# Performance work log

Hardware: AMD Instinct MI355X
Metric: run time of the kernel (lower is better)

Reference implementation:

```python
import jax, jax.numpy as jnp
import numpy as np

N_NODES = 100000
N_EDGES = 1600000
IN_F = 128
H_F = 128
N_CLS = 8
N_LAYERS = 6


def setup_inputs() -> dict:
    key = jax.random.key(0)
    ks = jax.random.split(key, 8)
    scale = 1.0 / np.sqrt(H_F)
    return {
        "in_feat": jax.random.normal(ks[0], (N_NODES, IN_F), dtype=jnp.float32),
        "src": jax.random.randint(ks[1], (N_EDGES,), 0, N_NODES, dtype=jnp.int32),
        "dst": jax.random.randint(ks[2], (N_EDGES,), 0, N_NODES, dtype=jnp.int32),
        "edge_weight": jax.random.uniform(ks[3], (N_EDGES,), dtype=jnp.float32),
        "conv_W": jax.random.normal(ks[4], (N_LAYERS, H_F, H_F), dtype=jnp.float32) * scale,
        "conv_b": jnp.zeros((N_LAYERS, H_F), dtype=jnp.float32),
        "lin_W": jax.random.normal(ks[5], (H_F, N_CLS), dtype=jnp.float32) * scale,
        "lin_b": jnp.zeros((N_CLS,), dtype=jnp.float32),
    }


def _degree_norms(src, dst, n):
    ones = jnp.ones(src.shape[0], dtype=jnp.float32)
    out_deg = jax.ops.segment_sum(ones, src, num_segments=n)
    in_deg = jax.ops.segment_sum(ones, dst, num_segments=n)
    # DGL norm='both': clamp degrees to min 1, then ^-0.5 (structural degrees)
    norm_src = jnp.power(jnp.maximum(out_deg, 1.0), -0.5)[:, None]  # [N,1]
    norm_dst = jnp.power(jnp.maximum(in_deg, 1.0), -0.5)[:, None]   # [N,1]
    return norm_src, norm_dst


def _graph_conv(x, W, b, src, dst, ew, norm_src, norm_dst):
    # linear commutes with (linear) aggregation; apply weight first
    h = (x @ W) * norm_src                     # [N,F]
    msg = h[src] * ew[:, None]                 # [E,F] gather * edge weight
    agg = jax.ops.segment_sum(msg, dst, num_segments=x.shape[0])
    return agg * norm_dst + b


def reference(in_feat, src, dst, edge_weight, conv_W, conv_b, lin_W, lin_b):
    norm_src, norm_dst = _degree_norms(src, dst, in_feat.shape[0])
    h = in_feat
    for i in range(N_LAYERS):
        h = jax.nn.leaky_relu(
            _graph_conv(h, conv_W[i], conv_b[i], src, dst, edge_weight, norm_src, norm_dst),
            negative_slope=0.01,
        )
    return h @ lin_W + lin_b
```

## Files before the change

### kernel.cpp

```cpp
#include <hip/hip_runtime.h>
#include <math.h>

#define N_NODES 100000
#define N_EDGES 1600000
#define HF 128
#define N_CLS 8
#define N_LAYERS 6
#define TILE_N 64
#define SCAN_B 1024
#define SCAN_NB ((N_NODES + SCAN_B - 1) / SCAN_B)
#define HBINS 8192
#define HCHUNK ((N_NODES + HBINS - 1) / HBINS)
#define HSLICE 8

__global__ void deg_rank_kernel(const int* __restrict__ dst,
                                int* __restrict__ ind, int* __restrict__ rank) {
    int e = blockIdx.x * blockDim.x + threadIdx.x;
    if (e < N_EDGES) {
        rank[e] = atomicAdd(&ind[dst[e]], 1);
    }
}

__global__ __launch_bounds__(1024) void outdeg_hist_kernel(const int* __restrict__ src,
                                                           int* __restrict__ outd) {
    __shared__ int hist[HBINS];
    int chunk = blockIdx.x;
    int slice = blockIdx.y;
    int lo = chunk * HBINS;
    int hi = lo + HBINS;
    for (int i = threadIdx.x; i < HBINS; i += 1024) hist[i] = 0;
    __syncthreads();
    const int4* s4 = (const int4*)src;
    const int n4 = N_EDGES / 4;
    int per = (n4 + HSLICE - 1) / HSLICE;
    int beg = slice * per;
    int end = beg + per; if (end > n4) end = n4;
    for (int i = beg + threadIdx.x; i < end; i += 1024) {
        int4 v = s4[i];
        if (v.x >= lo && v.x < hi) atomicAdd(&hist[v.x - lo], 1);
        if (v.y >= lo && v.y < hi) atomicAdd(&hist[v.y - lo], 1);
        if (v.z >= lo && v.z < hi) atomicAdd(&hist[v.z - lo], 1);
        if (v.w >= lo && v.w < hi) atomicAdd(&hist[v.w - lo], 1);
    }
    __syncthreads();
    for (int i = threadIdx.x; i < HBINS; i += 1024) {
        int c = hist[i];
        if (c != 0 && lo + i < N_NODES) atomicAdd(&outd[lo + i], c);
    }
}

__global__ void norm_kernel(const int* __restrict__ outd, const int* __restrict__ ind,
                            float* __restrict__ ns, float* __restrict__ nd) {
    int n = blockIdx.x * blockDim.x + threadIdx.x;
    if (n < N_NODES) {
        int od = outd[n]; if (od < 1) od = 1;
        int id = ind[n];  if (id < 1) id = 1;
        ns[n] = rsqrtf((float)od);
        nd[n] = rsqrtf((float)id);
    }
}

__global__ __launch_bounds__(SCAN_B) void scan1_kernel(const int* __restrict__ deg,
                                                       int* __restrict__ incl,
                                                       int* __restrict__ bsum) {
    __shared__ int buf[SCAN_B];
    int t = threadIdx.x;
    int g = blockIdx.x * SCAN_B + t;
    int v = (g < N_NODES) ? deg[g] : 0;
    buf[t] = v;
    __syncthreads();
    #pragma unroll
    for (int off = 1; off < SCAN_B; off <<= 1) {
        int add = (t >= off) ? buf[t - off] : 0;
        __syncthreads();
        buf[t] += add;
        __syncthreads();
    }
    if (g < N_NODES) incl[g] = buf[t];
    if (t == SCAN_B - 1) bsum[blockIdx.x] = buf[t];
}

__global__ __launch_bounds__(128) void scan2_kernel(int* __restrict__ bsum) {
    __shared__ int buf[128];
    int t = threadIdx.x;
    buf[t] = (t < SCAN_NB) ? bsum[t] : 0;
    __syncthreads();
    #pragma unroll
    for (int off = 1; off < 128; off <<= 1) {
        int add = (t >= off) ? buf[t - off] : 0;
        __syncthreads();
        buf[t] += add;
        __syncthreads();
    }
    if (t < SCAN_NB) bsum[t] = buf[t];
}

__global__ __launch_bounds__(SCAN_B) void scan3_kernel(const int* __restrict__ deg,
                                                       const int* __restrict__ incl,
                                                       const int* __restrict__ bsum,
                                                       int* __restrict__ row_ptr) {
    int t = threadIdx.x;
    int g = blockIdx.x * SCAN_B + t;
    if (g < N_NODES) {
        int off = (blockIdx.x > 0) ? bsum[blockIdx.x - 1] : 0;
        row_ptr[g] = off + incl[g] - deg[g];
    }
    if (g == 0) row_ptr[N_NODES] = bsum[SCAN_NB - 1];
}

__global__ void scatter2_kernel(const int* __restrict__ src, const int* __restrict__ dst,
                                const float* __restrict__ ew, const float* __restrict__ ns,
                                const float* __restrict__ nd, const int* __restrict__ row_ptr,
                                const int* __restrict__ rank, float2* __restrict__ esw) {
    int e = blockIdx.x * blockDim.x + threadIdx.x;
    if (e < N_EDGES) {
        int s = src[e];
        int d = dst[e];
        int pos = row_ptr[d] + rank[e];
        esw[pos] = make_float2(__int_as_float(s), ew[e] * ns[s] * nd[d]);
    }
}

__global__ __launch_bounds__(256) void gemm_kernel(const float* __restrict__ X,
                                                   const float* __restrict__ W,
                                                   float* __restrict__ Y) {
    __shared__ float Xs[TILE_N][HF];
    int tid = threadIdx.x;
    int nodeBase = blockIdx.x * TILE_N;

    for (int i = tid; i < TILE_N * (HF / 4); i += 256) {
        int r = i >> 5;
        int c = i & 31;
        int n = nodeBase + r;
        float4 v = make_float4(0.f, 0.f, 0.f, 0.f);
        if (n < N_NODES) v = ((const float4*)(X + (size_t)n * HF))[c];
        ((float4*)(&Xs[r][0]))[c] = v;
    }
    __syncthreads();

    int tx = tid & 31;
    int ty = tid >> 5;

    float acc[8][4];
    #pragma unroll
    for (int i = 0; i < 8; i++)
        #pragma unroll
        for (int j = 0; j < 4; j++) acc[i][j] = 0.f;

    const float4* W4 = (const float4*)W;

    for (int k4 = 0; k4 < HF / 4; k4++) {
        float4 wv0 = W4[(k4 * 4 + 0) * 32 + tx];
        float4 wv1 = W4[(k4 * 4 + 1) * 32 + tx];
        float4 wv2 = W4[(k4 * 4 + 2) * 32 + tx];
        float4 wv3 = W4[(k4 * 4 + 3) * 32 + tx];
        #pragma unroll
        for (int i = 0; i < 8; i++) {
            float4 xv = ((const float4*)(&Xs[ty + 8 * i][0]))[k4];
            acc[i][0] += xv.x * wv0.x; acc[i][1] += xv.x * wv0.y;
            acc[i][2] += xv.x * wv0.z; acc[i][3] += xv.x * wv0.w;
            acc[i][0] += xv.y * wv1.x; acc[i][1] += xv.y * wv1.y;
            acc[i][2] += xv.y * wv1.z; acc[i][3] += xv.y * wv1.w;
            acc[i][0] += xv.z * wv2.x; acc[i][1] += xv.z * wv2.y;
            acc[i][2] += xv.z * wv2.z; acc[i][3] += xv.z * wv2.w;
            acc[i][0] += xv.w * wv3.x; acc[i][1] += xv.w * wv3.y;
            acc[i][2] += xv.w * wv3.z; acc[i][3] += xv.w * wv3.w;
        }
    }

    #pragma unroll
    for (int i = 0; i < 8; i++) {
        int n = nodeBase + ty + 8 * i;
        if (n < N_NODES) {
            float4 o = make_float4(acc[i][0], acc[i][1], acc[i][2], acc[i][3]);
            ((float4*)(Y + (size_t)n * HF))[tx] = o;
        }
    }
}

__global__ __launch_bounds__(256) void agg_kernel(const float* __restrict__ hl,
                                                  const int* __restrict__ row_ptr,
                                                  const float2* __restrict__ esw,
                                                  const float* __restrict__ bias,
                                                  float* __restrict__ out) {
    int node = blockIdx.x * 4 + (threadIdx.x >> 6);
    if (node >= N_NODES) return;
    int lane = threadIdx.x & 63;
    int half = lane >> 5;
    int fl = lane & 31;

    int beg = row_ptr[node];
    int end = row_ptr[node + 1];
    float ax = 0.f, ay = 0.f, az = 0.f, aw = 0.f;

    int i = beg;
    for (; i + 2 <= end; i += 2) {
        float2 p = esw[i + half];
        int s = __float_as_int(p.x);
        float4 v = ((const float4*)(hl + (size_t)s * HF))[fl];
        ax += v.x * p.y; ay += v.y * p.y;
        az += v.z * p.y; aw += v.w * p.y;
    }
    if (i < end && half == 0) {
        float2 p = esw[i];
        int s = __float_as_int(p.x);
        float4 v = ((const float4*)(hl + (size_t)s * HF))[fl];
        ax += v.x * p.y; ay += v.y * p.y;
        az += v.z * p.y; aw += v.w * p.y;
    }

    ax += __shfl_xor(ax, 32);
    ay += __shfl_xor(ay, 32);
    az += __shfl_xor(az, 32);
    aw += __shfl_xor(aw, 32);

    if (half == 0) {
        float4 bb = ((const float4*)bias)[fl];
        float ox = ax + bb.x;
        float oy = ay + bb.y;
        float oz = az + bb.z;
        float ow = aw + bb.w;
        ox = (ox > 0.f) ? ox : 0.01f * ox;
        oy = (oy > 0.f) ? oy : 0.01f * oy;
        oz = (oz > 0.f) ? oz : 0.01f * oz;
        ow = (ow > 0.f) ? ow : 0.01f * ow;
        ((float4*)(out + (size_t)node * HF))[fl] = make_float4(ox, oy, oz, ow);
    }
}

__global__ __launch_bounds__(256) void proj_kernel(const float* __restrict__ h,
                                                   const float* __restrict__ W,
                                                   const float* __restrict__ b,
                                                   float* __restrict__ out) {
    int node = blockIdx.x * (blockDim.x >> 6) + (threadIdx.x >> 6);
    if (node >= N_NODES) return;
    int lane = threadIdx.x & 63;

    float2 v = *(const float2*)(h + (size_t)node * HF + lane * 2);
    float acc[N_CLS];
    #pragma unroll
    for (int c = 0; c < N_CLS; c++) {
        acc[c] = v.x * W[(lane * 2) * N_CLS + c] + v.y * W[(lane * 2 + 1) * N_CLS + c];
    }
    #pragma unroll
    for (int off = 32; off > 0; off >>= 1) {
        #pragma unroll
        for (int c = 0; c < N_CLS; c++) acc[c] += __shfl_down(acc[c], off);
    }
    if (lane == 0) {
        #pragma unroll
        for (int c = 0; c < N_CLS; c++) out[(size_t)node * N_CLS + c] = acc[c] + b[c];
    }
}

extern "C" void kernel_launch(void* const* d_in, const int* in_sizes, int n_in,
                              void* d_out, int out_size, void* d_ws, size_t ws_size,
                              hipStream_t stream) {
    const float* in_feat = (const float*)d_in[0];
    const int*   src     = (const int*)d_in[1];
    const int*   dst     = (const int*)d_in[2];
    const float* ew      = (const float*)d_in[3];
    const float* conv_W  = (const float*)d_in[4];
    const float* conv_b  = (const float*)d_in[5];
    const float* lin_W   = (const float*)d_in[6];
    const float* lin_b   = (const float*)d_in[7];
    float* out = (float*)d_out;

    char* p = (char*)d_ws;
    float* hA = (float*)p;        p += (size_t)N_NODES * HF * sizeof(float);
    float* hB = (float*)p;        p += (size_t)N_NODES * HF * sizeof(float);
    float2* esw = (float2*)p;     p += (size_t)N_EDGES * sizeof(float2);
    int*   row_ptr = (int*)p;     p += ((size_t)N_NODES + 8) * sizeof(int);
    int*   out_deg = (int*)p;     p += (size_t)N_NODES * sizeof(int);
    int*   in_deg = (int*)p;      p += (size_t)N_NODES * sizeof(int);
    float* norm_src = (float*)p;  p += (size_t)N_NODES * sizeof(float);
    float* norm_dst = (float*)p;  p += (size_t)N_NODES * sizeof(float);
    int*   incl = (int*)p;        p += (size_t)N_NODES * sizeof(int);
    int*   bsum = (int*)p;        p += 256 * sizeof(int);
    int*   rank = (int*)hB;
    (void)p; (void)ws_size; (void)in_sizes; (void)n_in; (void)out_size;

    hipMemsetAsync(out_deg, 0, (size_t)N_NODES * sizeof(int), stream);
    hipMemsetAsync(in_deg, 0, (size_t)N_NODES * sizeof(int), stream);

    int egrid = (N_EDGES + 255) / 256;
    int ngrid = (N_NODES + 255) / 256;

    deg_rank_kernel<<<egrid, 256, 0, stream>>>(dst, in_deg, rank);
    outdeg_hist_kernel<<<dim3(HCHUNK, HSLICE), 1024, 0, stream>>>(src, out_deg);
    norm_kernel<<<ngrid, 256, 0, stream>>>(out_deg, in_deg, norm_src, norm_dst);
    scan1_kernel<<<SCAN_NB, SCAN_B, 0, stream>>>(in_deg, incl, bsum);
    scan2_kernel<<<1, 128, 0, stream>>>(bsum);
    scan3_kernel<<<SCAN_NB, SCAN_B, 0, stream>>>(in_deg, incl, bsum, row_ptr);
    scatter2_kernel<<<egrid, 256, 0, stream>>>(src, dst, ew, norm_src, norm_dst,
                                               row_ptr, rank, esw);

    int ggrid = (N_NODES + TILE_N - 1) / TILE_N;
    int agrid = (N_NODES + 3) / 4;

    const float* cur = in_feat;
    for (int l = 0; l < N_LAYERS; l++) {
        gemm_kernel<<<ggrid, 256, 0, stream>>>(cur, conv_W + (size_t)l * HF * HF, hB);
        agg_kernel<<<agrid, 256, 0, stream>>>(hB, row_ptr, esw,
                                              conv_b + (size_t)l * HF, hA);
        cur = hA;
    }
    proj_kernel<<<agrid, 256, 0, stream>>>(hA, lin_W, lin_b, out);
}
```

Baseline: 1.304 ms.

## Replace FP32 GEMM with bf16x3 split-precision MFMA matrix cores

The per-layer dense transform moves from scalar FP32 FMA to MFMA bf16 instructions. Each operand is split into three bf16 parts (hi/mid/lo) and six cross-product passes are accumulated to keep accuracy close to FP32. Weights are pre-split and transposed once by a new prep kernel, and activations are split on the fly into a swizzled shared-memory layout. This adds conversion work, triples the shared-memory footprint and writes output with scalar strided stores.

Measured after the change: 1.364 ms. 1.05x slower.

```diff
diff --git a/kernel.cpp b/kernel.cpp
--- a/kernel.cpp
+++ b/kernel.cpp
@@ -13,6 +13,20 @@
 #define HCHUNK ((N_NODES + HBINS - 1) / HBINS)
 #define HSLICE 8
 
+typedef __attribute__((ext_vector_type(8))) short bf16x8;
+typedef __attribute__((ext_vector_type(4))) float f32x4;
+
+__device__ __forceinline__ unsigned short bf_rne(float x) {
+    unsigned u = __float_as_uint(x);
+    u += 0x7FFFu + ((u >> 16) & 1u);
+    return (unsigned short)(u >> 16);
+}
+__device__ __forceinline__ float bf_to_f(unsigned short h) {
+    return __uint_as_float(((unsigned)h) << 16);
+}
+
+#define LDSOFF(row, k) (((row) << 8) + (((((k) >> 3) << 4) ^ (((row) & 7) << 4))) + (((k) & 7) << 1))
+
 __global__ void deg_rank_kernel(const int* __restrict__ dst,
                                 int* __restrict__ ind, int* __restrict__ rank) {
     int e = blockIdx.x * blockDim.x + threadIdx.x;
@@ -121,59 +135,109 @@
     }
 }
 
-__global__ __launch_bounds__(256) void gemm_kernel(const float* __restrict__ X,
-                                                   const float* __restrict__ W,
-                                                   float* __restrict__ Y) {
-    __shared__ float Xs[TILE_N][HF];
+__global__ __launch_bounds__(256) void wprep_kernel(const float* __restrict__ conv_W,
+                                                    unsigned short* __restrict__ wt) {
+    int l = blockIdx.y;
+    int idx = blockIdx.x * 256 + threadIdx.x;
+    int k = idx >> 7, f = idx & 127;
+    float x = conv_W[(size_t)l * 16384 + idx];
+    unsigned short h0 = bf_rne(x);
+    float r1 = x - bf_to_f(h0);
+    unsigned short h1 = bf_rne(r1);
+    float r2 = r1 - bf_to_f(h1);
+    unsigned short h2 = bf_rne(r2);
+    size_t base = (size_t)l * 3 * 16384 + (size_t)f * 128 + k;
+    wt[base]         = h0;
+    wt[base + 16384] = h1;
+    wt[base + 32768] = h2;
+}
+
+__global__ __launch_bounds__(256) void gemm_mfma_kernel(const float* __restrict__ X,
+                                                        const unsigned short* __restrict__ Wt,
+                                                        float* __restrict__ Y) {
+    __shared__ unsigned short Xb[3][TILE_N * HF];
     int tid = threadIdx.x;
     int nodeBase = blockIdx.x * TILE_N;
 
-    for (int i = tid; i < TILE_N * (HF / 4); i += 256) {
-        int r = i >> 5;
-        int c = i & 31;
+    for (int it = 0; it < 8; it++) {
+        int idx = tid + it * 256;
+        int r = idx >> 5;
+        int c = idx & 31;
         int n = nodeBase + r;
         float4 v = make_float4(0.f, 0.f, 0.f, 0.f);
         if (n < N_NODES) v = ((const float4*)(X + (size_t)n * HF))[c];
-        ((float4*)(&Xs[r][0]))[c] = v;
-    }
-    __syncthreads();
-
-    int tx = tid & 31;
-    int ty = tid >> 5;
-
-    float acc[8][4];
-    #pragma unroll
-    for (int i = 0; i < 8; i++)
-        #pragma unroll
-        for (int j = 0; j < 4; j++) acc[i][j] = 0.f;
-
-    const float4* W4 = (const float4*)W;
-
-    for (int k4 = 0; k4 < HF / 4; k4++) {
-        float4 wv0 = W4[(k4 * 4 + 0) * 32 + tx];
-        float4 wv1 = W4[(k4 * 4 + 1) * 32 + tx];
-        float4 wv2 = W4[(k4 * 4 + 2) * 32 + tx];
-        float4 wv3 = W4[(k4 * 4 + 3) * 32 + tx];
-        #pragma unroll
-        for (int i = 0; i < 8; i++) {
-            float4 xv = ((const float4*)(&Xs[ty + 8 * i][0]))[k4];
-            acc[i][0] += xv.x * wv0.x; acc[i][1] += xv.x * wv0.y;
-            acc[i][2] += xv.x * wv0.z; acc[i][3] += xv.x * wv0.w;
-            acc[i][0] += xv.y * wv1.x; acc[i][1] += xv.y * wv1.y;
-            acc[i][2] += xv.y * wv1.z; acc[i][3] += xv.y * wv1.w;
-            acc[i][0] += xv.z * wv2.x; acc[i][1] += xv.z * wv2.y;
-            acc[i][2] += xv.z * wv2.z; acc[i][3] += xv.z * wv2.w;
-            acc[i][0] += xv.w * wv3.x; acc[i][1] += xv.w * wv3.y;
-            acc[i][2] += xv.w * wv3.z; acc[i][3] += xv.w * wv3.w;
+        float vv[4] = {v.x, v.y, v.z, v.w};
+        unsigned short h0[4], h1[4], h2[4];
+        #pragma unroll
+        for (int j = 0; j < 4; j++) {
+            float x = vv[j];
+            h0[j] = bf_rne(x);
+            float r1 = x - bf_to_f(h0[j]);
+            h1[j] = bf_rne(r1);
+            float r2 = r1 - bf_to_f(h1[j]);
+            h2[j] = bf_rne(r2);
         }
-    }
-
-    #pragma unroll
-    for (int i = 0; i < 8; i++) {
-        int n = nodeBase + ty + 8 * i;
-        if (n < N_NODES) {
-            float4 o = make_float4(acc[i][0], acc[i][1], acc[i][2], acc[i][3]);
-            ((float4*)(Y + (size_t)n * HF))[tx] = o;
+        int boff = LDSOFF(r, c * 4) >> 1;
+        *(uint2*)&Xb[0][boff] = *(uint2*)h0;
+        *(uint2*)&Xb[1][boff] = *(uint2*)h1;
+        *(uint2*)&Xb[2][boff] = *(uint2*)h2;
+    }
+    __syncthreads();
+
+    int lane = tid & 63;
+    int wv = tid >> 6;
+    int lrow = lane & 15;
+    int lk8 = lane >> 4;
+
+    f32x4 acc[4][2];
+    #pragma unroll
+    for (int m = 0; m < 4; m++)
+        #pragma unroll
+        for (int n = 0; n < 2; n++)
+            acc[m][n] = (f32x4){0.f, 0.f, 0.f, 0.f};
+
+    const int pa[6] = {0, 0, 1, 0, 1, 2};
+    const int pb[6] = {0, 1, 0, 2, 1, 0};
+
+    #pragma unroll
+    for (int p = 0; p < 6; p++) {
+        const unsigned short* xb = Xb[pa[p]];
+        const unsigned short* wb = Wt + (size_t)pb[p] * 16384;
+        #pragma unroll
+        for (int ks = 0; ks < 4; ks++) {
+            int k0 = ks * 32 + lk8 * 8;
+            bf16x8 afr[4];
+            #pragma unroll
+            for (int m = 0; m < 4; m++) {
+                int row = m * 16 + lrow;
+                afr[m] = *(const bf16x8*)&xb[LDSOFF(row, k0) >> 1];
+            }
+            bf16x8 bfr[2];
+            #pragma unroll
+            for (int n = 0; n < 2; n++) {
+                int col = wv * 32 + n * 16 + lrow;
+                bfr[n] = *(const bf16x8*)&wb[col * 128 + k0];
+            }
+            #pragma unroll
+            for (int m = 0; m < 4; m++)
+                #pragma unroll
+                for (int n = 0; n < 2; n++)
+                    acc[m][n] = __builtin_amdgcn_mfma_f32_16x16x32_bf16(
+                        afr[m], bfr[n], acc[m][n], 0, 0, 0);
+        }
+    }
+
+    #pragma unroll
+    for (int m = 0; m < 4; m++) {
+        int rowBase = nodeBase + m * 16 + lk8 * 4;
+        #pragma unroll
+        for (int n = 0; n < 2; n++) {
+            int feat = wv * 32 + n * 16 + lrow;
+            #pragma unroll
+            for (int rr = 0; rr < 4; rr++) {
+                int nd = rowBase + rr;
+                if (nd < N_NODES) Y[(size_t)nd * HF + feat] = acc[m][n][rr];
+            }
         }
     }
 }
@@ -277,6 +341,7 @@
     float* norm_dst = (float*)p;  p += (size_t)N_NODES * sizeof(float);
     int*   incl = (int*)p;        p += (size_t)N_NODES * sizeof(int);
     int*   bsum = (int*)p;        p += 256 * sizeof(int);
+    unsigned short* wt = (unsigned short*)p; p += (size_t)N_LAYERS * 3 * 16384 * sizeof(unsigned short);
     int*   rank = (int*)hB;
     (void)p; (void)ws_size; (void)in_sizes; (void)n_in; (void)out_size;
 
@@ -294,13 +359,14 @@
     scan3_kernel<<<SCAN_NB, SCAN_B, 0, stream>>>(in_deg, incl, bsum, row_ptr);
     scatter2_kernel<<<egrid, 256, 0, stream>>>(src, dst, ew, norm_src, norm_dst,
                                                row_ptr, rank, esw);
+    wprep_kernel<<<dim3(64, N_LAYERS), 256, 0, stream>>>(conv_W, wt);
 
     int ggrid = (N_NODES + TILE_N - 1) / TILE_N;
     int agrid = (N_NODES + 3) / 4;
 
     const float* cur = in_feat;
     for (int l = 0; l < N_LAYERS; l++) {
-        gemm_kernel<<<ggrid, 256, 0, stream>>>(cur, conv_W + (size_t)l * HF * HF, hB);
+        gemm_mfma_kernel<<<ggrid, 256, 0, stream>>>(cur, wt + (size_t)l * 3 * 16384, hB);
         agg_kernel<<<agrid, 256, 0, stream>>>(hB, row_ptr, esw,
                                               conv_b + (size_t)l * HF, hA);
         cur = hA;
```

## Sub-bin CSR edges by source range to improve gather locality

Applied to the files above, without the earlier changes.

Edges in each destination row are now bucketed into 16 bins by source-node range, using a counting sort over N_NODES*16 bins, so each node's neighbors are visited roughly in ascending source order. The aim is better L2 locality for the feature gathers in the aggregation kernel across all six layers. In exchange the preprocessing scan grows sixteenfold (1.6M bins, with a serial chunked second-level scan), and bins and incl reuse the hA buffer.

After: 1.336 ms. 2.5% more time.

```diff
diff --git a/kernel.cpp b/kernel.cpp
--- a/kernel.cpp
+++ b/kernel.cpp
@@ -7,17 +7,23 @@
 #define N_CLS 8
 #define N_LAYERS 6
 #define TILE_N 64
+#define NS 16
+#define SDIV 6250
+#define NBINS (N_NODES * NS)
 #define SCAN_B 1024
-#define SCAN_NB ((N_NODES + SCAN_B - 1) / SCAN_B)
+#define SCAN_NB1 ((NBINS + SCAN_B - 1) / SCAN_B)
 #define HBINS 8192
 #define HCHUNK ((N_NODES + HBINS - 1) / HBINS)
 #define HSLICE 8
 
-__global__ void deg_rank_kernel(const int* __restrict__ dst,
-                                int* __restrict__ ind, int* __restrict__ rank) {
+__global__ void deg_rank_kernel(const int* __restrict__ src, const int* __restrict__ dst,
+                                int* __restrict__ bins, int* __restrict__ rank) {
     int e = blockIdx.x * blockDim.x + threadIdx.x;
     if (e < N_EDGES) {
-        rank[e] = atomicAdd(&ind[dst[e]], 1);
+        int s = src[e];
+        int d = dst[e];
+        int bin = d * NS + s / SDIV;
+        rank[e] = atomicAdd(&bins[bin], 1);
     }
 }
 
@@ -49,12 +55,13 @@
     }
 }
 
-__global__ void norm_kernel(const int* __restrict__ outd, const int* __restrict__ ind,
+__global__ void norm_kernel(const int* __restrict__ outd, const int* __restrict__ sptr,
                             float* __restrict__ ns, float* __restrict__ nd) {
     int n = blockIdx.x * blockDim.x + threadIdx.x;
     if (n < N_NODES) {
         int od = outd[n]; if (od < 1) od = 1;
-        int id = ind[n];  if (id < 1) id = 1;
+        int id = sptr[(n + 1) * NS] - sptr[n * NS];
+        if (id < 1) id = 1;
         ns[n] = rsqrtf((float)od);
         nd[n] = rsqrtf((float)id);
     }
@@ -66,7 +73,7 @@
     __shared__ int buf[SCAN_B];
     int t = threadIdx.x;
     int g = blockIdx.x * SCAN_B + t;
-    int v = (g < N_NODES) ? deg[g] : 0;
+    int v = (g < NBINS) ? deg[g] : 0;
     buf[t] = v;
     __syncthreads();
     #pragma unroll
@@ -76,47 +83,58 @@
         buf[t] += add;
         __syncthreads();
     }
-    if (g < N_NODES) incl[g] = buf[t];
+    if (g < NBINS) incl[g] = buf[t];
     if (t == SCAN_B - 1) bsum[blockIdx.x] = buf[t];
 }
 
-__global__ __launch_bounds__(128) void scan2_kernel(int* __restrict__ bsum) {
-    __shared__ int buf[128];
+__global__ __launch_bounds__(1024) void scan2_kernel(int* __restrict__ bsum) {
+    __shared__ int buf[1024];
+    __shared__ int carry_s;
     int t = threadIdx.x;
-    buf[t] = (t < SCAN_NB) ? bsum[t] : 0;
-    __syncthreads();
-    #pragma unroll
-    for (int off = 1; off < 128; off <<= 1) {
-        int add = (t >= off) ? buf[t - off] : 0;
-        __syncthreads();
-        buf[t] += add;
-        __syncthreads();
-    }
-    if (t < SCAN_NB) bsum[t] = buf[t];
+    if (t == 0) carry_s = 0;
+    __syncthreads();
+    for (int base = 0; base < SCAN_NB1; base += 1024) {
+        int v = (base + t < SCAN_NB1) ? bsum[base + t] : 0;
+        buf[t] = v;
+        __syncthreads();
+        #pragma unroll
+        for (int off = 1; off < 1024; off <<= 1) {
+            int add = (t >= off) ? buf[t - off] : 0;
+            __syncthreads();
+            buf[t] += add;
+            __syncthreads();
+        }
+        int incl = buf[t];
+        int carry = carry_s;
+        if (base + t < SCAN_NB1) bsum[base + t] = carry + incl;
+        __syncthreads();
+        if (t == 1023) carry_s = carry + incl;
+        __syncthreads();
+    }
 }
 
 __global__ __launch_bounds__(SCAN_B) void scan3_kernel(const int* __restrict__ deg,
                                                        const int* __restrict__ incl,
                                                        const int* __restrict__ bsum,
-                                                       int* __restrict__ row_ptr) {
+                                                       int* __restrict__ sptr) {
     int t = threadIdx.x;
     int g = blockIdx.x * SCAN_B + t;
-    if (g < N_NODES) {
+    if (g < NBINS) {
         int off = (blockIdx.x > 0) ? bsum[blockIdx.x - 1] : 0;
-        row_ptr[g] = off + incl[g] - deg[g];
-    }
-    if (g == 0) row_ptr[N_NODES] = bsum[SCAN_NB - 1];
+        sptr[g] = off + incl[g] - deg[g];
+    }
+    if (g == 0) sptr[NBINS] = bsum[SCAN_NB1 - 1];
 }
 
 __global__ void scatter2_kernel(const int* __restrict__ src, const int* __restrict__ dst,
                                 const float* __restrict__ ew, const float* __restrict__ ns,
-                                const float* __restrict__ nd, const int* __restrict__ row_ptr,
+                                const float* __restrict__ nd, const int* __restrict__ sptr,
                                 const int* __restrict__ rank, float2* __restrict__ esw) {
     int e = blockIdx.x * blockDim.x + threadIdx.x;
     if (e < N_EDGES) {
         int s = src[e];
         int d = dst[e];
-        int pos = row_ptr[d] + rank[e];
+        int pos = sptr[d * NS + s / SDIV] + rank[e];
         esw[pos] = make_float2(__int_as_float(s), ew[e] * ns[s] * nd[d]);
     }
 }
@@ -179,7 +197,7 @@
 }
 
 __global__ __launch_bounds__(256) void agg_kernel(const float* __restrict__ hl,
-                                                  const int* __restrict__ row_ptr,
+                                                  const int* __restrict__ sptr,
                                                   const float2* __restrict__ esw,
                                                   const float* __restrict__ bias,
                                                   float* __restrict__ out) {
@@ -189,8 +207,8 @@
     int half = lane >> 5;
     int fl = lane & 31;
 
-    int beg = row_ptr[node];
-    int end = row_ptr[node + 1];
+    int beg = sptr[node * NS];
+    int end = sptr[node * NS + NS];
     float ax = 0.f, ay = 0.f, az = 0.f, aw = 0.f;
 
     int i = beg;
@@ -270,30 +288,31 @@
     float* hA = (float*)p;        p += (size_t)N_NODES * HF * sizeof(float);
     float* hB = (float*)p;        p += (size_t)N_NODES * HF * sizeof(float);
     float2* esw = (float2*)p;     p += (size_t)N_EDGES * sizeof(float2);
-    int*   row_ptr = (int*)p;     p += ((size_t)N_NODES + 8) * sizeof(int);
+    int*   sptr = (int*)p;        p += ((size_t)NBINS + 8) * sizeof(int);
+    int*   bsum = (int*)p;        p += ((size_t)SCAN_NB1 + 8) * sizeof(int);
     int*   out_deg = (int*)p;     p += (size_t)N_NODES * sizeof(int);
-    int*   in_deg = (int*)p;      p += (size_t)N_NODES * sizeof(int);
     float* norm_src = (float*)p;  p += (size_t)N_NODES * sizeof(float);
     float* norm_dst = (float*)p;  p += (size_t)N_NODES * sizeof(float);
-    int*   incl = (int*)p;        p += (size_t)N_NODES * sizeof(int);
-    int*   bsum = (int*)p;        p += 256 * sizeof(int);
-    int*   rank = (int*)hB;
     (void)p; (void)ws_size; (void)in_sizes; (void)n_in; (void)out_size;
 
+    int* rank = (int*)hB;
+    int* bins = (int*)hA;
+    int* incl = (int*)hA + 2000000;
+
+    hipMemsetAsync(bins, 0, (size_t)NBINS * sizeof(int), stream);
     hipMemsetAsync(out_deg, 0, (size_t)N_NODES * sizeof(int), stream);
-    hipMemsetAsync(in_deg, 0, (size_t)N_NODES * sizeof(int), stream);
 
     int egrid = (N_EDGES + 255) / 256;
     int ngrid = (N_NODES + 255) / 256;
 
-    deg_rank_kernel<<<egrid, 256, 0, stream>>>(dst, in_deg, rank);
+    deg_rank_kernel<<<egrid, 256, 0, stream>>>(src, dst, bins, rank);
     outdeg_hist_kernel<<<dim3(HCHUNK, HSLICE), 1024, 0, stream>>>(src, out_deg);
-    norm_kernel<<<ngrid, 256, 0, stream>>>(out_deg, in_deg, norm_src, norm_dst);
-    scan1_kernel<<<SCAN_NB, SCAN_B, 0, stream>>>(in_deg, incl, bsum);
-    scan2_kernel<<<1, 128, 0, stream>>>(bsum);
-    scan3_kernel<<<SCAN_NB, SCAN_B, 0, stream>>>(in_deg, incl, bsum, row_ptr);
+    scan1_kernel<<<SCAN_NB1, SCAN_B, 0, stream>>>(bins, incl, bsum);
+    scan2_kernel<<<1, 1024, 0, stream>>>(bsum);
+    scan3_kernel<<<SCAN_NB1, SCAN_B, 0, stream>>>(bins, incl, bsum, sptr);
+    norm_kernel<<<ngrid, 256, 0, stream>>>(out_deg, sptr, norm_src, norm_dst);
     scatter2_kernel<<<egrid, 256, 0, stream>>>(src, dst, ew, norm_src, norm_dst,
-                                               row_ptr, rank, esw);
+                                               sptr, rank, esw);
 
     int ggrid = (N_NODES + TILE_N - 1) / TILE_N;
     int agrid = (N_NODES + 3) / 4;
@@ -301,7 +320,7 @@
     const float* cur = in_feat;
     for (int l = 0; l < N_LAYERS; l++) {
         gemm_kernel<<<ggrid, 256, 0, stream>>>(cur, conv_W + (size_t)l * HF * HF, hB);
-        agg_kernel<<<agrid, 256, 0, stream>>>(hB, row_ptr, esw,
+        agg_kernel<<<agrid, 256, 0, stream>>>(hB, sptr, esw,
                                               conv_b + (size_t)l * HF, hA);
         cur = hA;
     }
```

## Replace tiled shared-memory GEMM with register-resident weight column kernel

Applied to the files above, without the earlier changes.

The per-layer dense transform now keeps one column of the weight matrix in registers per thread. Waves stream node rows from global memory, computing one output feature per thread with a persistent grid of fixed blocks. This removes the shared-memory staging and synchronization of X tiles and the repeated W reloads. In exchange it issues many more per-node global loads, has low FMA per load, and needs around 128 registers for weights, which limits occupancy.

After: 2.542 ms. 94.9% more time.

```diff
diff --git a/kernel.cpp b/kernel.cpp
--- a/kernel.cpp
+++ b/kernel.cpp
@@ -6,12 +6,13 @@
 #define HF 128
 #define N_CLS 8
 #define N_LAYERS 6
-#define TILE_N 64
 #define SCAN_B 1024
 #define SCAN_NB ((N_NODES + SCAN_B - 1) / SCAN_B)
 #define HBINS 8192
 #define HCHUNK ((N_NODES + HBINS - 1) / HBINS)
 #define HSLICE 8
+#define GEMM_BLOCKS 768
+#define GEMM_PER ((N_NODES + GEMM_BLOCKS - 1) / GEMM_BLOCKS)
 
 __global__ void deg_rank_kernel(const int* __restrict__ dst,
                                 int* __restrict__ ind, int* __restrict__ rank) {
@@ -121,60 +122,33 @@
     }
 }
 
-__global__ __launch_bounds__(256) void gemm_kernel(const float* __restrict__ X,
-                                                   const float* __restrict__ W,
-                                                   float* __restrict__ Y) {
-    __shared__ float Xs[TILE_N][HF];
+__global__ __launch_bounds__(256) void gemm_wreg_kernel(const float* __restrict__ X,
+                                                        const float* __restrict__ W,
+                                                        float* __restrict__ Y) {
     int tid = threadIdx.x;
-    int nodeBase = blockIdx.x * TILE_N;
-
-    for (int i = tid; i < TILE_N * (HF / 4); i += 256) {
-        int r = i >> 5;
-        int c = i & 31;
-        int n = nodeBase + r;
-        float4 v = make_float4(0.f, 0.f, 0.f, 0.f);
-        if (n < N_NODES) v = ((const float4*)(X + (size_t)n * HF))[c];
-        ((float4*)(&Xs[r][0]))[c] = v;
-    }
-    __syncthreads();
-
-    int tx = tid & 31;
-    int ty = tid >> 5;
-
-    float acc[8][4];
-    #pragma unroll
-    for (int i = 0; i < 8; i++)
+    int w = tid >> 6;
+    int lane = tid & 63;
+    int f = (w & 1) * 64 + lane;
+
+    float wr[HF];
+    #pragma unroll
+    for (int k = 0; k < HF; k++) wr[k] = W[k * HF + f];
+
+    int start = blockIdx.x * GEMM_PER;
+    int end = start + GEMM_PER; if (end > N_NODES) end = N_NODES;
+
+    for (int node = start + (w >> 1); node < end; node += 2) {
+        const float4* xr = (const float4*)(X + (size_t)node * HF);
+        float a0 = 0.f, a1 = 0.f, a2 = 0.f, a3 = 0.f;
         #pragma unroll
-        for (int j = 0; j < 4; j++) acc[i][j] = 0.f;
-
-    const float4* W4 = (const float4*)W;
-
-    for (int k4 = 0; k4 < HF / 4; k4++) {
-        float4 wv0 = W4[(k4 * 4 + 0) * 32 + tx];
-        float4 wv1 = W4[(k4 * 4 + 1) * 32 + tx];
-        float4 wv2 = W4[(k4 * 4 + 2) * 32 + tx];
-        float4 wv3 = W4[(k4 * 4 + 3) * 32 + tx];
-        #pragma unroll
-        for (int i = 0; i < 8; i++) {
-            float4 xv = ((const float4*)(&Xs[ty + 8 * i][0]))[k4];
-            acc[i][0] += xv.x * wv0.x; acc[i][1] += xv.x * wv0.y;
-            acc[i][2] += xv.x * wv0.z; acc[i][3] += xv.x * wv0.w;
-            acc[i][0] += xv.y * wv1.x; acc[i][1] += xv.y * wv1.y;
-            acc[i][2] += xv.y * wv1.z; acc[i][3] += xv.y * wv1.w;
-            acc[i][0] += xv.z * wv2.x; acc[i][1] += xv.z * wv2.y;
-            acc[i][2] += xv.z * wv2.z; acc[i][3] += xv.z * wv2.w;
-            acc[i][0] += xv.w * wv3.x; acc[i][1] += xv.w * wv3.y;
-            acc[i][2] += xv.w * wv3.z; acc[i][3] += xv.w * wv3.w;
+        for (int k4 = 0; k4 < HF / 4; k4++) {
+            float4 xq = xr[k4];
+            a0 += xq.x * wr[k4 * 4 + 0];
+            a1 += xq.y * wr[k4 * 4 + 1];
+            a2 += xq.z * wr[k4 * 4 + 2];
+            a3 += xq.w * wr[k4 * 4 + 3];
         }
-    }
-
-    #pragma unroll
-    for (int i = 0; i < 8; i++) {
-        int n = nodeBase + ty + 8 * i;
-        if (n < N_NODES) {
-            float4 o = make_float4(acc[i][0], acc[i][1], acc[i][2], acc[i][3]);
-            ((float4*)(Y + (size_t)n * HF))[tx] = o;
-        }
+        Y[(size_t)node * HF + f] = (a0 + a1) + (a2 + a3);
     }
 }
 
@@ -295,12 +269,11 @@
     scatter2_kernel<<<egrid, 256, 0, stream>>>(src, dst, ew, norm_src, norm_dst,
                                                row_ptr, rank, esw);
 
-    int ggrid = (N_NODES + TILE_N - 1) / TILE_N;
     int agrid = (N_NODES + 3) / 4;
 
     const float* cur = in_feat;
     for (int l = 0; l < N_LAYERS; l++) {
-        gemm_kernel<<<ggrid, 256, 0, stream>>>(cur, conv_W + (size_t)l * HF * HF, hB);
+        gemm_wreg_kernel<<<GEMM_BLOCKS, 256, 0, stream>>>(cur, conv_W + (size_t)l * HF * HF, hB);
         agg_kernel<<<agrid, 256, 0, stream>>>(hB, row_ptr, esw,
                                               conv_b + (size_t)l * HF, hA);
         cur = hA;
```
